# Optimization experiments

Measured on AMD Instinct MI355X. Metric: run time of the kernel, lower is better.

The kernel has to match this reference:

```python
import jax, jax.numpy as jnp
import numpy as np

B, MAXN, F, H, T, L = 32, 1024, 215, 256, 8, 3
N = B * MAXN            # 32768 global nodes
E = 524288              # total edges, global indices


def setup_inputs() -> dict:
    key = jax.random.key(0)
    ks = jax.random.split(key, 12)
    s = 0.05
    return {
        "node_features": jax.random.normal(ks[0], (B, MAXN, F), dtype=jnp.float32),
        "edge_index": jax.random.randint(ks[1], (2, E), 0, N, dtype=jnp.int32),
        "edge_type": jax.random.randint(ks[2], (E,), 0, T, dtype=jnp.int32),
        # input projection
        "Wp": jax.random.normal(ks[3], (H, F), dtype=jnp.float32) * s,
        "bp": jax.random.normal(ks[4], (H,), dtype=jnp.float32) * s,
        # per-layer, per-edge-type message linears
        "Wm": jax.random.normal(ks[5], (L, T, H, H), dtype=jnp.float32) * s,
        "bm": jax.random.normal(ks[6], (L, T, H), dtype=jnp.float32) * s,
        # per-layer GRUCell params (torch layout: [r|z|n] stacked, 3H rows)
        "Wih": jax.random.normal(ks[7], (L, 3 * H, H), dtype=jnp.float32) * s,
        "Whh": jax.random.normal(ks[8], (L, 3 * H, H), dtype=jnp.float32) * s,
        "bih": jax.random.normal(ks[9], (L, 3 * H), dtype=jnp.float32) * s,
        "bhh": jax.random.normal(ks[10], (L, 3 * H), dtype=jnp.float32) * s,
    }


def _gru_cell(x, h, Wih, Whh, bih, bhh):
    # torch.nn.GRUCell math
    gi = x @ Wih.T + bih            # (N, 3H)
    gh = h @ Whh.T + bhh            # (N, 3H)
    i_r, i_z, i_n = jnp.split(gi, 3, axis=-1)
    h_r, h_z, h_n = jnp.split(gh, 3, axis=-1)
    r = jax.nn.sigmoid(i_r + h_r)
    z = jax.nn.sigmoid(i_z + h_z)
    n = jnp.tanh(i_n + r * h_n)
    return (1.0 - z) * n + z * h


def reference(node_features, edge_index, edge_type, Wp, bp, Wm, bm, Wih, Whh, bih, bhh):
    # flatten batch of graphs into global node array, project to hidden
    h = node_features.reshape(-1, F) @ Wp.T + bp          # (N, H)
    src, dst = edge_index[0], edge_index[1]
    for l in range(L):
        # apply all T type-specific linears to every node once (equivalent to
        # the per-edge-type mask+gather+Linear loop), then gather per edge
        Ht = jnp.einsum('nd,ted->nte', h, Wm[l]) + bm[l]  # (N, T, H)
        msg = Ht[src, edge_type]                           # (E, H) gather
        m = jax.ops.segment_sum(msg, dst, num_segments=N)  # scatter-add (N, H)
        h = _gru_cell(m, h, Wih[l], Whh[l], bih[l], bhh[l])
        # dropout is identity in eval mode
    # readout: full graphs -> sum each graph's node block
    return h.reshape(B, MAXN, H).sum(axis=1)               # (B, H)
```

## Files before the change

kernel.cpp:

```cpp
#include <hip/hip_runtime.h>

#define N_NODES 32768
#define E_EDGES 524288
#define F_IN    215
#define H_DIM   256
#define T_TYPES 8
#define L_LAYERS 3
#define B_GRAPHS 32
#define MAXN_   1024
#define NT_BINS (N_NODES * T_TYPES)

typedef float  f32x4  __attribute__((ext_vector_type(4)));
typedef __bf16 bf16x8 __attribute__((ext_vector_type(8)));

__device__ __forceinline__ unsigned short f2bf(float f) {
  union { float f; unsigned u; } v; v.f = f;
  unsigned r = v.u + 0x7fffu + ((v.u >> 16) & 1u);
  return (unsigned short)(r >> 16);
}
__device__ __forceinline__ float bf2f(unsigned short h) {
  union { unsigned u; float f; } v; v.u = ((unsigned)h) << 16;
  return v.f;
}
__device__ __forceinline__ float bflo(unsigned u) { union { unsigned x; float f; } v; v.x = u << 16; return v.f; }
__device__ __forceinline__ float bfhi(unsigned u) { union { unsigned x; float f; } v; v.x = u & 0xffff0000u; return v.f; }

typedef const __attribute__((address_space(1))) unsigned int* gas_ptr;
typedef __attribute__((address_space(3))) unsigned int* las_ptr;
__device__ __forceinline__ void gload_lds16(const unsigned short* g, unsigned short* l) {
  __builtin_amdgcn_global_load_lds((gas_ptr)g, (las_ptr)l, 16, 0, 0);
}

static constexpr size_t OFF_BIG     = 0;
static constexpr size_t REL_CURSOR  = 1048576;
static constexpr size_t REL_BSUM    = 2097152;
static constexpr size_t REL_WPPAD   = 33554432;
static constexpr size_t REL_HALT    = 50331648;
static constexpr size_t OFF_H_B     = 134217728;
static constexpr size_t OFF_M_B     = 150994944;
static constexpr size_t OFF_WMB     = 167772160;
static constexpr size_t OFF_WIH     = 170917888;
static constexpr size_t OFF_WHH     = 172097536;
static constexpr size_t OFF_OFFS    = 173277184;
static constexpr size_t OFF_SORTED  = 174326016;
static constexpr size_t OFF_CNT     = 175374592;
static constexpr size_t WS_REQUIRED = 175898880;

__global__ void hist_kernel(const int* __restrict__ dst, const int* __restrict__ et,
                            int* __restrict__ cnt) {
  int e = blockIdx.x * 256 + threadIdx.x;
  atomicAdd(&cnt[dst[e] * T_TYPES + et[e]], 1);
}

__global__ void cvt_cnt16(const int* __restrict__ counts, unsigned short* __restrict__ c16) {
  int i = blockIdx.x * 256 + threadIdx.x;
  c16[i] = (unsigned short)counts[i];
}

__global__ __launch_bounds__(1024) void scan1(const int* __restrict__ cnt,
                                              int* __restrict__ offs,
                                              int* __restrict__ bsum) {
  __shared__ int wsum[16];
  const int t = threadIdx.x, lane = t & 63, wid = t >> 6;
  const int idx = blockIdx.x * 1024 + t;
  const int v = cnt[idx];
  int x = v;
  #pragma unroll
  for (int off = 1; off < 64; off <<= 1) {
    int u = __shfl_up(x, off, 64);
    if (lane >= off) x += u;
  }
  if (lane == 63) wsum[wid] = x;
  __syncthreads();
  int wbase = 0;
  for (int i = 0; i < wid; ++i) wbase += wsum[i];
  offs[idx] = wbase + x - v;
  if (t == 1023) bsum[blockIdx.x] = wbase + x;
}

__global__ __launch_bounds__(256) void scan2(int* __restrict__ bsum) {
  __shared__ int wsum[4];
  const int t = threadIdx.x, lane = t & 63, wid = t >> 6;
  const int v = bsum[t];
  int x = v;
  #pragma unroll
  for (int off = 1; off < 64; off <<= 1) {
    int u = __shfl_up(x, off, 64);
    if (lane >= off) x += u;
  }
  if (lane == 63) wsum[wid] = x;
  __syncthreads();
  int wbase = 0;
  for (int i = 0; i < wid; ++i) wbase += wsum[i];
  __syncthreads();
  bsum[t] = wbase + x - v;
}

__global__ __launch_bounds__(1024) void scan3(int* __restrict__ offs,
                                              const int* __restrict__ bsum,
                                              int* __restrict__ cursor) {
  const int idx = blockIdx.x * 1024 + threadIdx.x;
  const int o = offs[idx] + bsum[blockIdx.x];
  offs[idx] = o;
  cursor[idx] = o;
  if (idx == 0) offs[NT_BINS] = E_EDGES;
}

__global__ void reorder_kernel(const int* __restrict__ src, const int* __restrict__ dst,
                               const int* __restrict__ et, int* __restrict__ cursor,
                               unsigned short* __restrict__ sorted) {
  int e = blockIdx.x * 256 + threadIdx.x;
  int key = dst[e] * T_TYPES + et[e];
  int p = atomicAdd(&cursor[key], 1);
  sorted[p] = (unsigned short)src[e];
}

__global__ void cvt_f32_bf16(const float* __restrict__ in, unsigned short* __restrict__ out, int n) {
  int i = blockIdx.x * 256 + threadIdx.x;
  if (i < n) out[i] = f2bf(in[i]);
}

__global__ void pad_cvt(const float* __restrict__ in, unsigned short* __restrict__ out,
                        int rows, int cin) {
  int i = blockIdx.x * 256 + threadIdx.x;
  if (i >= rows * 256) return;
  int r = i >> 8, c = i & 255;
  out[i] = (c < cin) ? f2bf(in[(size_t)r * cin + c]) : (unsigned short)0;
}

__global__ __launch_bounds__(256, 2) void gemm_bt(
    const unsigned short* __restrict__ A,
    const unsigned short* __restrict__ W,
    const float* __restrict__ bias,
    unsigned short* __restrict__ C,
    int M, int K) {
  __shared__ unsigned short As[128 * 32];
  __shared__ unsigned short Bs[128 * 32];
  const int tid = threadIdx.x;
  const int lane = tid & 63;
  const int wv = tid >> 6;
  const int lrow = lane & 15;
  const int lquad = lane >> 4;
  const int bm0 = blockIdx.x * 128;
  const int bn0 = blockIdx.y * 128;
  const int srow = wv * 16 + (lane >> 2);
  const int scol = (lane & 3) * 8;

  f32x4 acc[2][8] = {};

  for (int kt = 0; kt < K; kt += 32) {
    #pragma unroll
    for (int i = 0; i < 2; ++i) {
      const int row = srow + i * 64;
      gload_lds16(A + (size_t)(bm0 + row) * K + kt + scol, &As[row * 32 + scol]);
      gload_lds16(W + (size_t)(bn0 + row) * K + kt + scol, &Bs[row * 32 + scol]);
    }
    __syncthreads();
    bf16x8 af[2], bfr[8];
    #pragma unroll
    for (int mt = 0; mt < 2; ++mt)
      af[mt] = *(const bf16x8*)(&As[(wv * 32 + mt * 16 + lrow) * 32 + lquad * 8]);
    #pragma unroll
    for (int nt = 0; nt < 8; ++nt)
      bfr[nt] = *(const bf16x8*)(&Bs[(nt * 16 + lrow) * 32 + lquad * 8]);
    #pragma unroll
    for (int mt = 0; mt < 2; ++mt)
      #pragma unroll
      for (int nt = 0; nt < 8; ++nt)
        acc[mt][nt] = __builtin_amdgcn_mfma_f32_16x16x32_bf16(af[mt], bfr[nt], acc[mt][nt], 0, 0, 0);
    __syncthreads();
  }

  #pragma unroll
  for (int mt = 0; mt < 2; ++mt) {
    #pragma unroll
    for (int r = 0; r < 4; ++r) {
      const int grow = bm0 + wv * 32 + mt * 16 + lquad * 4 + r;
      #pragma unroll
      for (int nt = 0; nt < 8; ++nt) {
        const int gcol = bn0 + nt * 16 + lrow;
        float v = acc[mt][nt][r] + (bias ? bias[gcol] : 0.f);
        C[(size_t)grow * M + gcol] = f2bf(v);
      }
    }
  }
}

__global__ __launch_bounds__(256, 2) void msg_gemm(
    const int* __restrict__ offs, const unsigned short* __restrict__ sorted,
    const unsigned short* __restrict__ hb, const unsigned short* __restrict__ Wt_l,
    const unsigned short* __restrict__ cnt16, const float* __restrict__ bm_l,
    unsigned short* __restrict__ m) {
  __shared__ unsigned short Ss[8 * 32 * 40];
  __shared__ unsigned short Bs[256 * 32];
  const int tid = threadIdx.x;
  const int lane = tid & 63;
  const int wv = tid >> 6;
  const int lrow = lane & 15;
  const int lquad = lane >> 4;
  const int wrow = wv & 1;
  const int wcol = wv >> 1;
  const int bm0 = blockIdx.x * 32;
  const int srow = wv * 16 + (lane >> 2);
  const int scol = (lane & 3) * 8;

  f32x4 acc[8] = {};

  for (int t = 0; t < T_TYPES; ++t) {
    #pragma unroll
    for (int step = 0; step < 2; ++step) {
      const int dloc = wv * 8 + step * 4 + lquad;
      const int bin = (bm0 + dloc) * T_TYPES + t;
      const int beg = offs[bin], end = offs[bin + 1];
      float a[16];
      #pragma unroll
      for (int j = 0; j < 16; ++j) a[j] = 0.f;
      int e = beg;
      for (; e + 2 <= end; e += 2) {
        const int s0 = sorted[e], s1 = sorted[e + 1];
        const unsigned short* h0 = hb + (size_t)s0 * H_DIM + lrow * 16;
        const unsigned short* h1 = hb + (size_t)s1 * H_DIM + lrow * 16;
        const uint4 v0 = *(const uint4*)h0;
        const uint4 w0 = *(const uint4*)(h0 + 8);
        const uint4 v1 = *(const uint4*)h1;
        const uint4 w1 = *(const uint4*)(h1 + 8);
        a[0]  += bflo(v0.x) + bflo(v1.x); a[1]  += bfhi(v0.x) + bfhi(v1.x);
        a[2]  += bflo(v0.y) + bflo(v1.y); a[3]  += bfhi(v0.y) + bfhi(v1.y);
        a[4]  += bflo(v0.z) + bflo(v1.z); a[5]  += bfhi(v0.z) + bfhi(v1.z);
        a[6]  += bflo(v0.w) + bflo(v1.w); a[7]  += bfhi(v0.w) + bfhi(v1.w);
        a[8]  += bflo(w0.x) + bflo(w1.x); a[9]  += bfhi(w0.x) + bfhi(w1.x);
        a[10] += bflo(w0.y) + bflo(w1.y); a[11] += bfhi(w0.y) + bfhi(w1.y);
        a[12] += bflo(w0.z) + bflo(w1.z); a[13] += bfhi(w0.z) + bfhi(w1.z);
        a[14] += bflo(w0.w) + bflo(w1.w); a[15] += bfhi(w0.w) + bfhi(w1.w);
      }
      if (e < end) {
        const int s0 = sorted[e];
        const unsigned short* h0 = hb + (size_t)s0 * H_DIM + lrow * 16;
        const uint4 v0 = *(const uint4*)h0;
        const uint4 w0 = *(const uint4*)(h0 + 8);
        a[0]  += bflo(v0.x); a[1]  += bfhi(v0.x);
        a[2]  += bflo(v0.y); a[3]  += bfhi(v0.y);
        a[4]  += bflo(v0.z); a[5]  += bfhi(v0.z);
        a[6]  += bflo(v0.w); a[7]  += bfhi(v0.w);
        a[8]  += bflo(w0.x); a[9]  += bfhi(w0.x);
        a[10] += bflo(w0.y); a[11] += bfhi(w0.y);
        a[12] += bflo(w0.z); a[13] += bfhi(w0.z);
        a[14] += bflo(w0.w); a[15] += bfhi(w0.w);
      }
      union { unsigned short us[16]; uint4 q[2]; } ob;
      #pragma unroll
      for (int j = 0; j < 16; ++j) ob.us[j] = f2bf(a[j]);
      uint4* p = (uint4*)&Ss[(lrow >> 1) * 1280 + dloc * 40 + (lrow & 1) * 16];
      p[0] = ob.q[0];
      p[1] = ob.q[1];
    }
    __syncthreads();
    const unsigned short* Wt = Wt_l + (size_t)t * 256 * 256;
    for (int kc = 0; kc < 8; ++kc) {
      #pragma unroll
      for (int i = 0; i < 4; ++i) {
        const int j = srow + i * 64;
        gload_lds16(Wt + (size_t)j * 256 + kc * 32 + scol, &Bs[j * 32 + scol]);
      }
      __syncthreads();
      const bf16x8 af = *(const bf16x8*)(&Ss[kc * 1280 + (wrow * 16 + lrow) * 40 + lquad * 8]);
      #pragma unroll
      for (int nt = 0; nt < 8; ++nt) {
        const bf16x8 bfr = *(const bf16x8*)(&Bs[((wcol * 8 + nt) * 16 + lrow) * 32 + lquad * 8]);
        acc[nt] = __builtin_amdgcn_mfma_f32_16x16x32_bf16(af, bfr, acc[nt], 0, 0, 0);
      }
      __syncthreads();
    }
  }

  float* bmS = (float*)Bs;
  for (int i = tid; i < T_TYPES * H_DIM; i += 256) bmS[i] = bm_l[i];
  __syncthreads();
  float cnt[4][8];
  #pragma unroll
  for (int r = 0; r < 4; ++r) {
    const int grow = bm0 + wrow * 16 + lquad * 4 + r;
    const uint4 cv = *(const uint4*)(cnt16 + (size_t)grow * T_TYPES);
    cnt[r][0] = (float)(cv.x & 0xffff); cnt[r][1] = (float)(cv.x >> 16);
    cnt[r][2] = (float)(cv.y & 0xffff); cnt[r][3] = (float)(cv.y >> 16);
    cnt[r][4] = (float)(cv.z & 0xffff); cnt[r][5] = (float)(cv.z >> 16);
    cnt[r][6] = (float)(cv.w & 0xffff); cnt[r][7] = (float)(cv.w >> 16);
  }
  #pragma unroll
  for (int nt = 0; nt < 8; ++nt) {
    const int gcol = wcol * 128 + nt * 16 + lrow;
    float bmv[8];
    #pragma unroll
    for (int t = 0; t < 8; ++t) bmv[t] = bmS[t * H_DIM + gcol];
    #pragma unroll
    for (int r = 0; r < 4; ++r) {
      const int grow = bm0 + wrow * 16 + lquad * 4 + r;
      float v = acc[nt][r];
      #pragma unroll
      for (int t = 0; t < 8; ++t) v += cnt[r][t] * bmv[t];
      m[(size_t)grow * H_DIM + gcol] = f2bf(v);
    }
  }
}

__global__ __launch_bounds__(256, 2) void gru_fused(
    const unsigned short* __restrict__ mB,
    const unsigned short* __restrict__ hin,
    const unsigned short* __restrict__ wih_l,
    const unsigned short* __restrict__ whh_l,
    const float* __restrict__ bih_l,
    const float* __restrict__ bhh_l,
    unsigned short* __restrict__ hout) {
  __shared__ unsigned short Am[64 * 32];
  __shared__ unsigned short Ah[64 * 32];
  __shared__ unsigned short Bs[384 * 32];
  const int tid = threadIdx.x;
  const int lane = tid & 63;
  const int wv = tid >> 6;
  const int lrow = lane & 15;
  const int lquad = lane >> 4;
  const int n0 = blockIdx.x * 64;
  const int c0 = blockIdx.y * 64;
  const int arow = tid >> 2;
  const int scol = (tid & 3) * 8;

  f32x4 acc[6][4] = {};

  for (int kt = 0; kt < 256; kt += 32) {
    gload_lds16(mB  + (size_t)(n0 + arow) * 256 + kt + scol, &Am[arow * 32 + scol]);
    gload_lds16(hin + (size_t)(n0 + arow) * 256 + kt + scol, &Ah[arow * 32 + scol]);
    #pragma unroll
    for (int g = 0; g < 3; ++g) {
      gload_lds16(wih_l + (size_t)(g * 256 + c0 + arow) * 256 + kt + scol,
                  &Bs[(g * 64 + arow) * 32 + scol]);
      gload_lds16(whh_l + (size_t)(g * 256 + c0 + arow) * 256 + kt + scol,
                  &Bs[((g + 3) * 64 + arow) * 32 + scol]);
    }
    __syncthreads();
    const bf16x8 am = *(const bf16x8*)(&Am[(wv * 16 + lrow) * 32 + lquad * 8]);
    const bf16x8 ah = *(const bf16x8*)(&Ah[(wv * 16 + lrow) * 32 + lquad * 8]);
    #pragma unroll
    for (int g = 0; g < 6; ++g) {
      const bf16x8 a = (g < 3) ? am : ah;
      #pragma unroll
      for (int nt = 0; nt < 4; ++nt) {
        const bf16x8 b = *(const bf16x8*)(&Bs[(g * 64 + nt * 16 + lrow) * 32 + lquad * 8]);
        acc[g][nt] = __builtin_amdgcn_mfma_f32_16x16x32_bf16(a, b, acc[g][nt], 0, 0, 0);
      }
    }
    __syncthreads();
  }

  #pragma unroll
  for (int nt = 0; nt < 4; ++nt) {
    const int c = c0 + nt * 16 + lrow;
    const float b_ir = bih_l[c], b_iz = bih_l[256 + c], b_in = bih_l[512 + c];
    const float b_hr = bhh_l[c], b_hz = bhh_l[256 + c], b_hn = bhh_l[512 + c];
    #pragma unroll
    for (int r = 0; r < 4; ++r) {
      const int node = n0 + wv * 16 + lquad * 4 + r;
      const float i_r = acc[0][nt][r] + b_ir;
      const float i_z = acc[1][nt][r] + b_iz;
      const float i_n = acc[2][nt][r] + b_in;
      const float h_r = acc[3][nt][r] + b_hr;
      const float h_z = acc[4][nt][r] + b_hz;
      const float h_n = acc[5][nt][r] + b_hn;
      const float rr = 1.f / (1.f + __expf(-(i_r + h_r)));
      const float zz = 1.f / (1.f + __expf(-(i_z + h_z)));
      const float nn = tanhf(i_n + rr * h_n);
      const float hp = bf2f(hin[(size_t)node * 256 + c]);
      hout[(size_t)node * 256 + c] = f2bf((1.f - zz) * nn + zz * hp);
    }
  }
}

__global__ __launch_bounds__(256) void readout_partial(const unsigned short* __restrict__ hb,
                                                       float* __restrict__ part) {
  const int b = blockIdx.x >> 3;
  const int ch = blockIdx.x & 7;
  const int c = threadIdx.x;
  const unsigned short* base = hb + ((size_t)b * MAXN_ + ch * 128) * H_DIM + c;
  float s = 0.f;
  #pragma unroll 4
  for (int i = 0; i < 128; ++i) s += bf2f(base[(size_t)i * H_DIM]);
  part[(size_t)blockIdx.x * H_DIM + c] = s;
}

__global__ __launch_bounds__(256) void readout_final(const float* __restrict__ part,
                                                     float* __restrict__ out) {
  const int b = blockIdx.x;
  const int c = threadIdx.x;
  float s = 0.f;
  #pragma unroll
  for (int i = 0; i < 8; ++i) s += part[((size_t)b * 8 + i) * H_DIM + c];
  out[b * H_DIM + c] = s;
}

extern "C" void kernel_launch(void* const* d_in, const int* in_sizes, int n_in,
                              void* d_out, int out_size, void* d_ws, size_t ws_size,
                              hipStream_t stream) {
  if (ws_size < WS_REQUIRED) return;

  const float* X   = (const float*)d_in[0];
  const int*   ei  = (const int*)d_in[1];
  const int*   et  = (const int*)d_in[2];
  const float* Wp  = (const float*)d_in[3];
  const float* bp  = (const float*)d_in[4];
  const float* Wm  = (const float*)d_in[5];
  const float* bm  = (const float*)d_in[6];
  const float* Wih = (const float*)d_in[7];
  const float* Whh = (const float*)d_in[8];
  const float* bih = (const float*)d_in[9];
  const float* bhh = (const float*)d_in[10];
  float* out = (float*)d_out;
  char* ws = (char*)d_ws;

  int*            counts = (int*)(ws + OFF_BIG);
  int*            cursor = (int*)(ws + OFF_BIG + REL_CURSOR);
  int*            bsum   = (int*)(ws + OFF_BIG + REL_BSUM);
  unsigned short* xpad   = (unsigned short*)(ws + OFF_BIG);
  unsigned short* wppad  = (unsigned short*)(ws + OFF_BIG + REL_WPPAD);
  unsigned short* h_alt  = (unsigned short*)(ws + OFF_BIG + REL_HALT);
  float*          part   = (float*)(ws + OFF_BIG);
  unsigned short* h_b    = (unsigned short*)(ws + OFF_H_B);
  unsigned short* m_b    = (unsigned short*)(ws + OFF_M_B);
  unsigned short* wmb    = (unsigned short*)(ws + OFF_WMB);
  unsigned short* wih_b  = (unsigned short*)(ws + OFF_WIH);
  unsigned short* whh_b  = (unsigned short*)(ws + OFF_WHH);
  int*            offs   = (int*)(ws + OFF_OFFS);
  unsigned short* sorted = (unsigned short*)(ws + OFF_SORTED);
  unsigned short* cnt16  = (unsigned short*)(ws + OFF_CNT);

  const int* src = ei;
  const int* dst = ei + E_EDGES;

  hipMemsetAsync(counts, 0, NT_BINS * sizeof(int), stream);
  hist_kernel<<<E_EDGES / 256, 256, 0, stream>>>(dst, et, counts);
  cvt_cnt16<<<NT_BINS / 256, 256, 0, stream>>>(counts, cnt16);
  scan1<<<NT_BINS / 1024, 1024, 0, stream>>>(counts, offs, bsum);
  scan2<<<1, 256, 0, stream>>>(bsum);
  scan3<<<NT_BINS / 1024, 1024, 0, stream>>>(offs, bsum, cursor);
  reorder_kernel<<<E_EDGES / 256, 256, 0, stream>>>(src, dst, et, cursor, sorted);

  pad_cvt<<<(N_NODES * 256) / 256, 256, 0, stream>>>(X, xpad, N_NODES, F_IN);
  pad_cvt<<<(256 * 256) / 256, 256, 0, stream>>>(Wp, wppad, 256, F_IN);
  cvt_f32_bf16<<<(L_LAYERS * T_TYPES * H_DIM * H_DIM) / 256, 256, 0, stream>>>(
      Wm, wmb, L_LAYERS * T_TYPES * H_DIM * H_DIM);
  cvt_f32_bf16<<<(L_LAYERS * 3 * H_DIM * H_DIM) / 256, 256, 0, stream>>>(Wih, wih_b, L_LAYERS * 3 * H_DIM * H_DIM);
  cvt_f32_bf16<<<(L_LAYERS * 3 * H_DIM * H_DIM) / 256, 256, 0, stream>>>(Whh, whh_b, L_LAYERS * 3 * H_DIM * H_DIM);

  gemm_bt<<<dim3(N_NODES / 128, 2), 256, 0, stream>>>(xpad, wppad, bp, h_b, H_DIM, 256);

  for (int l = 0; l < L_LAYERS; ++l) {
    const unsigned short* wm_l  = wmb + (size_t)l * T_TYPES * H_DIM * H_DIM;
    const unsigned short* wih_l = wih_b + (size_t)l * 3 * H_DIM * H_DIM;
    const unsigned short* whh_l = whh_b + (size_t)l * 3 * H_DIM * H_DIM;
    const float* bm_l  = bm + (size_t)l * T_TYPES * H_DIM;
    const float* bih_l = bih + (size_t)l * 3 * H_DIM;
    const float* bhh_l = bhh + (size_t)l * 3 * H_DIM;

    unsigned short* h_cur = (l & 1) ? h_alt : h_b;
    unsigned short* h_nxt = (l & 1) ? h_b : h_alt;

    msg_gemm<<<N_NODES / 32, 256, 0, stream>>>(offs, sorted, h_cur, wm_l, cnt16, bm_l, m_b);
    gru_fused<<<dim3(N_NODES / 64, 4), 256, 0, stream>>>(
        m_b, h_cur, wih_l, whh_l, bih_l, bhh_l, h_nxt);
  }

  readout_partial<<<B_GRAPHS * 8, 256, 0, stream>>>(h_alt, part);
  readout_final<<<B_GRAPHS, 256, 0, stream>>>(part, out);

  (void)in_sizes; (void)n_in; (void)out_size;
}
```

Baseline: 667.8 us.

## Drop LDS weight staging in msg and GRU GEMMs, widen msg_gemm to 512 threads

msg_gemm now runs 8 waves per 32-node block, with one destination node per lane quad, and reads the per-type weight fragments straight from global/L2 instead of staging them in LDS. It also derives per-bin counts from offs, so the cvt_cnt16 kernel and its buffer go away. gru_fused likewise loads Wih/Whh fragments into registers directly, with each wave covering all 64 rows, and its launch bounds rise to 3 blocks. The aim is to cut LDS traffic and barriers and to raise occupancy for the latency-bound gather, at the cost of more redundant global weight reads. offs and sorted move into the reused big scratch region to shrink the workspace.

```diff
diff --git a/kernel.cpp b/kernel.cpp
--- a/kernel.cpp
+++ b/kernel.cpp
@@ -36,25 +36,19 @@
 static constexpr size_t REL_BSUM    = 2097152;
 static constexpr size_t REL_WPPAD   = 33554432;
 static constexpr size_t REL_HALT    = 50331648;
+static constexpr size_t REL_OFFS    = 100663296;
+static constexpr size_t REL_SORTED  = 104857600;
 static constexpr size_t OFF_H_B     = 134217728;
 static constexpr size_t OFF_M_B     = 150994944;
 static constexpr size_t OFF_WMB     = 167772160;
 static constexpr size_t OFF_WIH     = 170917888;
 static constexpr size_t OFF_WHH     = 172097536;
-static constexpr size_t OFF_OFFS    = 173277184;
-static constexpr size_t OFF_SORTED  = 174326016;
-static constexpr size_t OFF_CNT     = 175374592;
-static constexpr size_t WS_REQUIRED = 175898880;
+static constexpr size_t WS_REQUIRED = 173277184;
 
 __global__ void hist_kernel(const int* __restrict__ dst, const int* __restrict__ et,
                             int* __restrict__ cnt) {
   int e = blockIdx.x * 256 + threadIdx.x;
   atomicAdd(&cnt[dst[e] * T_TYPES + et[e]], 1);
-}
-
-__global__ void cvt_cnt16(const int* __restrict__ counts, unsigned short* __restrict__ c16) {
-  int i = blockIdx.x * 256 + threadIdx.x;
-  c16[i] = (unsigned short)counts[i];
 }
 
 __global__ __launch_bounds__(1024) void scan1(const int* __restrict__ cnt,
@@ -186,13 +180,11 @@
   }
 }
 
-__global__ __launch_bounds__(256, 2) void msg_gemm(
+__global__ __launch_bounds__(512, 6) void msg_gemm(
     const int* __restrict__ offs, const unsigned short* __restrict__ sorted,
     const unsigned short* __restrict__ hb, const unsigned short* __restrict__ Wt_l,
-    const unsigned short* __restrict__ cnt16, const float* __restrict__ bm_l,
-    unsigned short* __restrict__ m) {
+    const float* __restrict__ bm_l, unsigned short* __restrict__ m) {
   __shared__ unsigned short Ss[8 * 32 * 40];
-  __shared__ unsigned short Bs[256 * 32];
   const int tid = threadIdx.x;
   const int lane = tid & 63;
   const int wv = tid >> 6;
@@ -201,15 +193,13 @@
   const int wrow = wv & 1;
   const int wcol = wv >> 1;
   const int bm0 = blockIdx.x * 32;
-  const int srow = wv * 16 + (lane >> 2);
-  const int scol = (lane & 3) * 8;
-
-  f32x4 acc[8] = {};
+  const int dloc = wv * 4 + lquad;
+
+  f32x4 acc[4] = {};
 
   for (int t = 0; t < T_TYPES; ++t) {
-    #pragma unroll
-    for (int step = 0; step < 2; ++step) {
-      const int dloc = wv * 8 + step * 4 + lquad;
+    __syncthreads();
+    {
       const int bin = (bm0 + dloc) * T_TYPES + t;
       const int beg = offs[bin], end = offs[bin + 1];
       float a[16];
@@ -218,12 +208,12 @@
       int e = beg;
       for (; e + 2 <= end; e += 2) {
         const int s0 = sorted[e], s1 = sorted[e + 1];
-        const unsigned short* h0 = hb + (size_t)s0 * H_DIM + lrow * 16;
-        const unsigned short* h1 = hb + (size_t)s1 * H_DIM + lrow * 16;
+        const unsigned short* h0 = hb + (size_t)s0 * H_DIM + lrow * 8;
+        const unsigned short* h1 = hb + (size_t)s1 * H_DIM + lrow * 8;
         const uint4 v0 = *(const uint4*)h0;
-        const uint4 w0 = *(const uint4*)(h0 + 8);
+        const uint4 w0 = *(const uint4*)(h0 + 128);
         const uint4 v1 = *(const uint4*)h1;
-        const uint4 w1 = *(const uint4*)(h1 + 8);
+        const uint4 w1 = *(const uint4*)(h1 + 128);
         a[0]  += bflo(v0.x) + bflo(v1.x); a[1]  += bfhi(v0.x) + bfhi(v1.x);
         a[2]  += bflo(v0.y) + bflo(v1.y); a[3]  += bfhi(v0.y) + bfhi(v1.y);
         a[4]  += bflo(v0.z) + bflo(v1.z); a[5]  += bfhi(v0.z) + bfhi(v1.z);
@@ -235,9 +225,9 @@
       }
       if (e < end) {
         const int s0 = sorted[e];
-        const unsigned short* h0 = hb + (size_t)s0 * H_DIM + lrow * 16;
+        const unsigned short* h0 = hb + (size_t)s0 * H_DIM + lrow * 8;
         const uint4 v0 = *(const uint4*)h0;
-        const uint4 w0 = *(const uint4*)(h0 + 8);
+        const uint4 w0 = *(const uint4*)(h0 + 128);
         a[0]  += bflo(v0.x); a[1]  += bfhi(v0.x);
         a[2]  += bflo(v0.y); a[3]  += bfhi(v0.y);
         a[4]  += bflo(v0.z); a[5]  += bfhi(v0.z);
@@ -250,48 +240,43 @@
       union { unsigned short us[16]; uint4 q[2]; } ob;
       #pragma unroll
       for (int j = 0; j < 16; ++j) ob.us[j] = f2bf(a[j]);
-      uint4* p = (uint4*)&Ss[(lrow >> 1) * 1280 + dloc * 40 + (lrow & 1) * 16];
-      p[0] = ob.q[0];
-      p[1] = ob.q[1];
-    }
-    __syncthreads();
-    const unsigned short* Wt = Wt_l + (size_t)t * 256 * 256;
+      const int chunkA = lrow >> 2;
+      const int offA = (lrow & 3) * 8;
+      *(uint4*)&Ss[chunkA * 1280 + dloc * 40 + offA] = ob.q[0];
+      *(uint4*)&Ss[(4 + chunkA) * 1280 + dloc * 40 + offA] = ob.q[1];
+    }
+    __syncthreads();
+    const unsigned short* Wt = Wt_l + (size_t)t * 65536;
+    #pragma unroll 2
     for (int kc = 0; kc < 8; ++kc) {
-      #pragma unroll
-      for (int i = 0; i < 4; ++i) {
-        const int j = srow + i * 64;
-        gload_lds16(Wt + (size_t)j * 256 + kc * 32 + scol, &Bs[j * 32 + scol]);
+      const bf16x8 af = *(const bf16x8*)(&Ss[kc * 1280 + (wrow * 16 + lrow) * 40 + lquad * 8]);
+      #pragma unroll
+      for (int nt = 0; nt < 4; ++nt) {
+        const int col = wcol * 64 + nt * 16 + lrow;
+        const bf16x8 b = *(const bf16x8*)(Wt + (size_t)col * 256 + kc * 32 + lquad * 8);
+        acc[nt] = __builtin_amdgcn_mfma_f32_16x16x32_bf16(af, b, acc[nt], 0, 0, 0);
       }
-      __syncthreads();
-      const bf16x8 af = *(const bf16x8*)(&Ss[kc * 1280 + (wrow * 16 + lrow) * 40 + lquad * 8]);
-      #pragma unroll
-      for (int nt = 0; nt < 8; ++nt) {
-        const bf16x8 bfr = *(const bf16x8*)(&Bs[((wcol * 8 + nt) * 16 + lrow) * 32 + lquad * 8]);
-        acc[nt] = __builtin_amdgcn_mfma_f32_16x16x32_bf16(af, bfr, acc[nt], 0, 0, 0);
-      }
-      __syncthreads();
-    }
-  }
-
-  float* bmS = (float*)Bs;
-  for (int i = tid; i < T_TYPES * H_DIM; i += 256) bmS[i] = bm_l[i];
-  __syncthreads();
+    }
+  }
+
   float cnt[4][8];
   #pragma unroll
   for (int r = 0; r < 4; ++r) {
     const int grow = bm0 + wrow * 16 + lquad * 4 + r;
-    const uint4 cv = *(const uint4*)(cnt16 + (size_t)grow * T_TYPES);
-    cnt[r][0] = (float)(cv.x & 0xffff); cnt[r][1] = (float)(cv.x >> 16);
-    cnt[r][2] = (float)(cv.y & 0xffff); cnt[r][3] = (float)(cv.y >> 16);
-    cnt[r][4] = (float)(cv.z & 0xffff); cnt[r][5] = (float)(cv.z >> 16);
-    cnt[r][6] = (float)(cv.w & 0xffff); cnt[r][7] = (float)(cv.w >> 16);
-  }
-  #pragma unroll
-  for (int nt = 0; nt < 8; ++nt) {
-    const int gcol = wcol * 128 + nt * 16 + lrow;
+    const int4 o0 = *(const int4*)(offs + grow * 8);
+    const int4 o1 = *(const int4*)(offs + grow * 8 + 4);
+    const int o8 = offs[grow * 8 + 8];
+    cnt[r][0] = (float)(o0.y - o0.x); cnt[r][1] = (float)(o0.z - o0.y);
+    cnt[r][2] = (float)(o0.w - o0.z); cnt[r][3] = (float)(o1.x - o0.w);
+    cnt[r][4] = (float)(o1.y - o1.x); cnt[r][5] = (float)(o1.z - o1.y);
+    cnt[r][6] = (float)(o1.w - o1.z); cnt[r][7] = (float)(o8 - o1.w);
+  }
+  #pragma unroll
+  for (int nt = 0; nt < 4; ++nt) {
+    const int gcol = wcol * 64 + nt * 16 + lrow;
     float bmv[8];
     #pragma unroll
-    for (int t = 0; t < 8; ++t) bmv[t] = bmS[t * H_DIM + gcol];
+    for (int t = 0; t < 8; ++t) bmv[t] = bm_l[t * H_DIM + gcol];
     #pragma unroll
     for (int r = 0; r < 4; ++r) {
       const int grow = bm0 + wrow * 16 + lquad * 4 + r;
@@ -303,7 +288,7 @@
   }
 }
 
-__global__ __launch_bounds__(256, 2) void gru_fused(
+__global__ __launch_bounds__(256, 3) void gru_fused(
     const unsigned short* __restrict__ mB,
     const unsigned short* __restrict__ hin,
     const unsigned short* __restrict__ wih_l,
@@ -313,7 +298,6 @@
     unsigned short* __restrict__ hout) {
   __shared__ unsigned short Am[64 * 32];
   __shared__ unsigned short Ah[64 * 32];
-  __shared__ unsigned short Bs[384 * 32];
   const int tid = threadIdx.x;
   const int lane = tid & 63;
   const int wv = tid >> 6;
@@ -327,44 +311,41 @@
   f32x4 acc[6][4] = {};
 
   for (int kt = 0; kt < 256; kt += 32) {
+    __syncthreads();
     gload_lds16(mB  + (size_t)(n0 + arow) * 256 + kt + scol, &Am[arow * 32 + scol]);
     gload_lds16(hin + (size_t)(n0 + arow) * 256 + kt + scol, &Ah[arow * 32 + scol]);
+    __syncthreads();
+    const int wr = c0 + wv * 16 + lrow;
+    bf16x8 bfr[6];
     #pragma unroll
     for (int g = 0; g < 3; ++g) {
-      gload_lds16(wih_l + (size_t)(g * 256 + c0 + arow) * 256 + kt + scol,
-                  &Bs[(g * 64 + arow) * 32 + scol]);
-      gload_lds16(whh_l + (size_t)(g * 256 + c0 + arow) * 256 + kt + scol,
-                  &Bs[((g + 3) * 64 + arow) * 32 + scol]);
-    }
-    __syncthreads();
-    const bf16x8 am = *(const bf16x8*)(&Am[(wv * 16 + lrow) * 32 + lquad * 8]);
-    const bf16x8 ah = *(const bf16x8*)(&Ah[(wv * 16 + lrow) * 32 + lquad * 8]);
-    #pragma unroll
-    for (int g = 0; g < 6; ++g) {
-      const bf16x8 a = (g < 3) ? am : ah;
-      #pragma unroll
-      for (int nt = 0; nt < 4; ++nt) {
-        const bf16x8 b = *(const bf16x8*)(&Bs[(g * 64 + nt * 16 + lrow) * 32 + lquad * 8]);
-        acc[g][nt] = __builtin_amdgcn_mfma_f32_16x16x32_bf16(a, b, acc[g][nt], 0, 0, 0);
-      }
-    }
-    __syncthreads();
-  }
-
-  #pragma unroll
-  for (int nt = 0; nt < 4; ++nt) {
-    const int c = c0 + nt * 16 + lrow;
-    const float b_ir = bih_l[c], b_iz = bih_l[256 + c], b_in = bih_l[512 + c];
-    const float b_hr = bhh_l[c], b_hz = bhh_l[256 + c], b_hn = bhh_l[512 + c];
+      bfr[g]     = *(const bf16x8*)(wih_l + (size_t)(g * 256 + wr) * 256 + kt + lquad * 8);
+      bfr[g + 3] = *(const bf16x8*)(whh_l + (size_t)(g * 256 + wr) * 256 + kt + lquad * 8);
+    }
+    #pragma unroll
+    for (int mt = 0; mt < 4; ++mt) {
+      const bf16x8 am = *(const bf16x8*)(&Am[(mt * 16 + lrow) * 32 + lquad * 8]);
+      const bf16x8 ah = *(const bf16x8*)(&Ah[(mt * 16 + lrow) * 32 + lquad * 8]);
+      #pragma unroll
+      for (int g = 0; g < 6; ++g)
+        acc[g][mt] = __builtin_amdgcn_mfma_f32_16x16x32_bf16(g < 3 ? am : ah, bfr[g], acc[g][mt], 0, 0, 0);
+    }
+  }
+
+  const int c = c0 + wv * 16 + lrow;
+  const float b_ir = bih_l[c], b_iz = bih_l[256 + c], b_in = bih_l[512 + c];
+  const float b_hr = bhh_l[c], b_hz = bhh_l[256 + c], b_hn = bhh_l[512 + c];
+  #pragma unroll
+  for (int mt = 0; mt < 4; ++mt) {
     #pragma unroll
     for (int r = 0; r < 4; ++r) {
-      const int node = n0 + wv * 16 + lquad * 4 + r;
-      const float i_r = acc[0][nt][r] + b_ir;
-      const float i_z = acc[1][nt][r] + b_iz;
-      const float i_n = acc[2][nt][r] + b_in;
-      const float h_r = acc[3][nt][r] + b_hr;
-      const float h_z = acc[4][nt][r] + b_hz;
-      const float h_n = acc[5][nt][r] + b_hn;
+      const int node = n0 + mt * 16 + lquad * 4 + r;
+      const float i_r = acc[0][mt][r] + b_ir;
+      const float i_z = acc[1][mt][r] + b_iz;
+      const float i_n = acc[2][mt][r] + b_in;
+      const float h_r = acc[3][mt][r] + b_hr;
+      const float h_z = acc[4][mt][r] + b_hz;
+      const float h_n = acc[5][mt][r] + b_hn;
       const float rr = 1.f / (1.f + __expf(-(i_r + h_r)));
       const float zz = 1.f / (1.f + __expf(-(i_z + h_z)));
       const float nn = tanhf(i_n + rr * h_n);
@@ -422,21 +403,19 @@
   unsigned short* wppad  = (unsigned short*)(ws + OFF_BIG + REL_WPPAD);
   unsigned short* h_alt  = (unsigned short*)(ws + OFF_BIG + REL_HALT);
   float*          part   = (float*)(ws + OFF_BIG);
+  int*            offs   = (int*)(ws + OFF_BIG + REL_OFFS);
+  unsigned short* sorted = (unsigned short*)(ws + OFF_BIG + REL_SORTED);
   unsigned short* h_b    = (unsigned short*)(ws + OFF_H_B);
   unsigned short* m_b    = (unsigned short*)(ws + OFF_M_B);
   unsigned short* wmb    = (unsigned short*)(ws + OFF_WMB);
   unsigned short* wih_b  = (unsigned short*)(ws + OFF_WIH);
   unsigned short* whh_b  = (unsigned short*)(ws + OFF_WHH);
-  int*            offs   = (int*)(ws + OFF_OFFS);
-  unsigned short* sorted = (unsigned short*)(ws + OFF_SORTED);
-  unsigned short* cnt16  = (unsigned short*)(ws + OFF_CNT);
 
   const int* src = ei;
   const int* dst = ei + E_EDGES;
 
   hipMemsetAsync(counts, 0, NT_BINS * sizeof(int), stream);
   hist_kernel<<<E_EDGES / 256, 256, 0, stream>>>(dst, et, counts);
-  cvt_cnt16<<<NT_BINS / 256, 256, 0, stream>>>(counts, cnt16);
   scan1<<<NT_BINS / 1024, 1024, 0, stream>>>(counts, offs, bsum);
   scan2<<<1, 256, 0, stream>>>(bsum);
   scan3<<<NT_BINS / 1024, 1024, 0, stream>>>(offs, bsum, cursor);
@@ -462,7 +441,7 @@
     unsigned short* h_cur = (l & 1) ? h_alt : h_b;
     unsigned short* h_nxt = (l & 1) ? h_b : h_alt;
 
-    msg_gemm<<<N_NODES / 32, 256, 0, stream>>>(offs, sorted, h_cur, wm_l, cnt16, bm_l, m_b);
+    msg_gemm<<<N_NODES / 32, 512, 0, stream>>>(offs, sorted, h_cur, wm_l, bm_l, m_b);
     gru_fused<<<dim3(N_NODES / 64, 4), 256, 0, stream>>>(
         m_b, h_cur, wih_l, whh_l, bih_l, bhh_l, h_nxt);
   }
```

Result: slower. 1.190 ms (+78.2%).
